# Performance work log

Hardware: AMD Instinct MI355X
Metric: run time of the kernel (lower is better)

The kernel has to match this reference:

```python
import jax, jax.numpy as jnp
import numpy as np

N = 50000      # nodes
E = 800000     # random edges (self loops appended in reference)
B = 500        # graphs
H = 4          # attention heads
F = 64         # feature_dim (per-head out channels)
SLOPE = 0.2    # GATConv leaky_relu negative slope


def gat_layer(x, src, dst, W, att_s, att_d, b):
    # x: [N, Fin]; W: [Fin, H*F]; att_s/att_d: [H, F]; b: [H*F]
    h = (x @ W).reshape(N, H, F)                       # [N,H,F]
    a_s = jnp.einsum('nhf,hf->nh', h, att_s)           # [N,H]
    a_d = jnp.einsum('nhf,hf->nh', h, att_d)           # [N,H]
    e = jax.nn.leaky_relu(a_s[src] + a_d[dst], SLOPE)  # [E',H]
    emax = jax.ops.segment_max(e, dst, num_segments=N) # [N,H] (finite: self loops)
    ee = jnp.exp(e - emax[dst])
    denom = jax.ops.segment_sum(ee, dst, num_segments=N)
    alpha = ee / denom[dst]                            # [E',H]
    out = jax.ops.segment_sum(alpha[:, :, None] * h[src], dst, num_segments=N)
    return out.reshape(N, H * F) + b


def setup_inputs() -> dict:
    key = jax.random.key(0)
    ks = jax.random.split(key, 32)
    s = 0.05
    inp = {
        'node_features': jax.random.normal(ks[0], (N, 5), jnp.float32),
        'building_mask': jax.random.randint(ks[1], (N,), 0, 2),
        'batch': jnp.sort(jax.random.randint(ks[2], (N,), 0, B)),
        'edge_index': jax.random.randint(ks[3], (2, E), 0, N),
        'bbox_W': jax.random.normal(ks[4], (5, 64)) * s,
        'bbox_b': jnp.zeros((64,), jnp.float32),
        'mask_embed': jax.random.normal(ks[5], (2, 64)) * s,
        'node_W': jax.random.normal(ks[6], (128, 64)) * s,
        'node_b': jnp.zeros((64,), jnp.float32),
        'w0': jax.random.normal(ks[7], (64, 256)) * s,
        'as0': jax.random.normal(ks[8], (H, F)) * s,
        'ad0': jax.random.normal(ks[9], (H, F)) * s,
        'b0': jnp.zeros((256,), jnp.float32),
        'w1': jax.random.normal(ks[10], (256, 256)) * s,
        'as1': jax.random.normal(ks[11], (H, F)) * s,
        'ad1': jax.random.normal(ks[12], (H, F)) * s,
        'b1': jnp.zeros((256,), jnp.float32),
        'w2': jax.random.normal(ks[13], (256, 256)) * s,
        'as2': jax.random.normal(ks[14], (H, F)) * s,
        'ad2': jax.random.normal(ks[15], (H, F)) * s,
        'b2': jnp.zeros((256,), jnp.float32),
        'agg_W': jax.random.normal(ks[16], (832, 256)) * s,
        'agg_b': jnp.zeros((256,), jnp.float32),
        'mu_W': jax.random.normal(ks[17], (256, 256)) * s,
        'mu_b': jnp.zeros((256,), jnp.float32),
        'var_W': jax.random.normal(ks[18], (256, 256)) * s,
        'var_b': jnp.zeros((256,), jnp.float32),
    }
    return inp


def reference(node_features, building_mask, batch, edge_index,
              bbox_W, bbox_b, mask_embed, node_W, node_b,
              w0, as0, ad0, b0, w1, as1, ad1, b1, w2, as2, ad2, b2,
              agg_W, agg_b, mu_W, mu_b, var_W, var_b):
    # node featurization
    x = jax.nn.relu(node_features @ bbox_W + bbox_b)          # [N,64]
    m = jax.nn.relu(mask_embed[building_mask])                 # [N,64]
    n0 = jax.nn.relu(jnp.concatenate([x, m], -1) @ node_W + node_b)  # [N,64]

    # self loops (GATConv add_self_loops=True)
    loop = jnp.arange(N, dtype=edge_index.dtype)
    src = jnp.concatenate([edge_index[0], loop])
    dst = jnp.concatenate([edge_index[1], loop])

    g = jax.ops.segment_max(n0, batch, num_segments=B, indices_are_sorted=True)
    g_embed = [g]

    n_t = jax.nn.relu(gat_layer(n0, src, dst, w0, as0, ad0, b0))
    g_embed.append(jax.ops.segment_max(n_t, batch, num_segments=B, indices_are_sorted=True))

    for (W, a_s, a_d, b) in [(w1, as1, ad1, b1), (w2, as2, ad2, b2)]:
        n_t = jax.nn.relu(gat_layer(n_t, src, dst, W, a_s, a_d, b))
        g_embed.append(jax.ops.segment_max(n_t, batch, num_segments=B, indices_are_sorted=True))

    latent = jnp.concatenate(g_embed, -1) @ agg_W + agg_b      # [B,256]
    mu = latent @ mu_W + mu_b
    log_var = latent @ var_W + var_b
    return (mu, log_var)
```

## Files before the change

### kernel.cpp

```cpp
#include <hip/hip_runtime.h>

#define NN 50000
#define EE 800000
#define BB 500
#define SCB 196

typedef short v8s __attribute__((ext_vector_type(8)));
typedef unsigned short v8u __attribute__((ext_vector_type(8)));
typedef float v4f __attribute__((ext_vector_type(4)));

__device__ __forceinline__ float bf2f(unsigned short u) {
    union { unsigned int i; float f; } v; v.i = ((unsigned int)u) << 16; return v.f;
}
__device__ __forceinline__ unsigned short f2bf(float f) {
    union { float f; unsigned int i; } v; v.f = f;
    unsigned int x = v.i;
    unsigned int r = (x + 0x7FFFu + ((x >> 16) & 1u)) >> 16;
    return (unsigned short)r;
}

__device__ __forceinline__ void gll16(const unsigned short* g, v8s* l) {
    __builtin_amdgcn_global_load_lds((const __attribute__((address_space(1))) unsigned int*)g,
                                     (__attribute__((address_space(3))) unsigned int*)l, 16, 0, 0);
}

__global__ void k_sentinel(float* out, float val) {
    int i = blockIdx.x * blockDim.x + threadIdx.x;
    if (i < BB * 512) out[i] = val;
}

__global__ void k_prep(const float* __restrict__ nf, const int* __restrict__ bmask,
                       const float* __restrict__ bboxW, const float* __restrict__ bboxb,
                       const float* __restrict__ membed, unsigned short* __restrict__ feat,
                       const float* __restrict__ a0, unsigned short* __restrict__ d0,
                       const float* __restrict__ a1, unsigned short* __restrict__ d1,
                       const float* __restrict__ a2, unsigned short* __restrict__ d2,
                       const float* __restrict__ a3, unsigned short* __restrict__ d3,
                       int* __restrict__ counts, float* __restrict__ gcat) {
    int g = blockIdx.x * blockDim.x + threadIdx.x;
    if (g < NN) counts[g] = 1;
    if (g < NN * 64) {
        int n = g >> 6, f = g & 63;
        float s = bboxb[f];
        for (int k = 0; k < 5; ++k) s += nf[n * 5 + k] * bboxW[k * 64 + f];
        s = fmaxf(s, 0.f);
        int bm = bmask[n]; if ((unsigned)bm > 1u) bm = 0;
        float mv = fmaxf(membed[bm * 64 + f], 0.f);
        feat[(size_t)n * 128 + f] = f2bf(s);
        feat[(size_t)n * 128 + 64 + f] = f2bf(mv);
        return;
    }
    g -= NN * 64;
    if (g >= 155648) {
        if (g < 155648 + BB * 768) {
            int idx = g - 155648;
            gcat[(idx / 768) * 832 + 64 + (idx % 768)] = 0.f;
        }
        return;
    }
    const float* in; unsigned short* out; int K, Nout, idx;
    if (g < 8192)        { in = a0; out = d0; K = 128; Nout = 64;  idx = g; }
    else if (g < 24576)  { in = a1; out = d1; K = 64;  Nout = 256; idx = g - 8192; }
    else if (g < 90112)  { in = a2; out = d2; K = 256; Nout = 256; idx = g - 24576; }
    else                 { in = a3; out = d3; K = 256; Nout = 256; idx = g - 90112; }
    int k = idx / Nout, n = idx % Nout;
    out[n * K + k] = f2bf(in[idx]);
}

template <int KT, bool BR, bool ATT, int GY>
__global__ __launch_bounds__(256) void k_gemm(const unsigned short* __restrict__ A,
                                              const unsigned short* __restrict__ Bt,
                                              const float* __restrict__ bias,
                                              unsigned short* __restrict__ C, int M, int ldc,
                                              const float* __restrict__ atts, const float* __restrict__ attd,
                                              float* __restrict__ asA, float* __restrict__ adA, int nbx) {
    constexpr int NT = KT / 64;
    constexpr int NB = (NT > 1) ? 2 : 1;
    __shared__ v8s As[NB][512];
    __shared__ v8s Bs[NB][512];
    __shared__ float ap[4][4][4][4][2];
    const int t = threadIdx.x;
    int bx, by;
    if (GY == 4) {
        int p = blockIdx.x;
        int gidx = p >> 5, r = p & 31;
        bx = gidx * 8 + (r & 7);
        by = r >> 3;
        if (bx >= nbx) return;
    } else {
        bx = blockIdx.x; by = 0;
    }
    const int m0 = bx * 64;
    const int n0g = by * 64;
    const int l = t & 63, w = t >> 6;
    const int q = l >> 4, r16 = l & 15;
    const int nloc = w * 16 + r16;

    const int roff0 = (w * 2 + 0) * 8 + (l >> 3);
    const int roff1 = (w * 2 + 1) * 8 + (l >> 3);
    const int kc = (l & 7) ^ (l >> 3);
    const unsigned short* Asrc0 = A + (size_t)(m0 + roff0) * KT + kc * 8;
    const unsigned short* Asrc1 = A + (size_t)(m0 + roff1) * KT + kc * 8;
    const unsigned short* Bsrc0 = Bt + (size_t)(n0g + roff0) * KT + kc * 8;
    const unsigned short* Bsrc1 = Bt + (size_t)(n0g + roff1) * KT + kc * 8;

    v4f acc[4];
#pragma unroll
    for (int i = 0; i < 4; ++i) acc[i] = (v4f){0.f, 0.f, 0.f, 0.f};

    gll16(Asrc0, &As[0][(w * 2 + 0) * 64]);
    gll16(Asrc1, &As[0][(w * 2 + 1) * 64]);
    gll16(Bsrc0, &Bs[0][(w * 2 + 0) * 64]);
    gll16(Bsrc1, &Bs[0][(w * 2 + 1) * 64]);
    __syncthreads();
#pragma unroll
    for (int kt = 0; kt < NT; ++kt) {
        const int b = kt & (NB - 1);
        if (kt + 1 < NT) {
            const int nb = (kt + 1) & (NB - 1);
            gll16(Asrc0 + (kt + 1) * 64, &As[nb][(w * 2 + 0) * 64]);
            gll16(Asrc1 + (kt + 1) * 64, &As[nb][(w * 2 + 1) * 64]);
            gll16(Bsrc0 + (kt + 1) * 64, &Bs[nb][(w * 2 + 0) * 64]);
            gll16(Bsrc1 + (kt + 1) * 64, &Bs[nb][(w * 2 + 1) * 64]);
        }
#pragma unroll
        for (int s = 0; s < 2; ++s) {
            int c = s * 4 + q;
            v8s bfr = Bs[b][nloc * 8 + (c ^ (nloc & 7))];
#pragma unroll
            for (int mt = 0; mt < 4; ++mt) {
                v8s afr = As[b][(mt * 16 + r16) * 8 + (c ^ (r16 & 7))];
                acc[mt] = __builtin_amdgcn_mfma_f32_16x16x32_bf16(afr, bfr, acc[mt], 0, 0, 0);
            }
        }
        __syncthreads();
    }

    const int col = n0g + nloc;
#pragma unroll
    for (int mt = 0; mt < 4; ++mt) {
#pragma unroll
        for (int r = 0; r < 4; ++r) {
            int row = m0 + mt * 16 + q * 4 + r;
            if (row < M) {
                float v = acc[mt][r];
                if (BR) v = fmaxf(v + bias[col], 0.f);
                C[(size_t)row * ldc + col] = f2bf(v);
            }
        }
    }
    if (ATT) {
        float sa = atts[n0g + nloc];
        float da = attd[n0g + nloc];
        float rs[4][4], rd[4][4];
#pragma unroll
        for (int mt = 0; mt < 4; ++mt)
#pragma unroll
            for (int r = 0; r < 4; ++r) { rs[mt][r] = acc[mt][r] * sa; rd[mt][r] = acc[mt][r] * da; }
#pragma unroll
        for (int d = 1; d < 16; d <<= 1) {
#pragma unroll
            for (int mt = 0; mt < 4; ++mt)
#pragma unroll
                for (int r = 0; r < 4; ++r) {
                    rs[mt][r] += __shfl_xor(rs[mt][r], d, 64);
                    rd[mt][r] += __shfl_xor(rd[mt][r], d, 64);
                }
        }
        if (r16 == 0) {
#pragma unroll
            for (int mt = 0; mt < 4; ++mt)
#pragma unroll
                for (int r = 0; r < 4; ++r) { ap[w][q][mt][r][0] = rs[mt][r]; ap[w][q][mt][r][1] = rd[mt][r]; }
        }
        __syncthreads();
        if (t < 128) {
            int row = t >> 1, which = t & 1;
            int qq = (row >> 2) & 3, mtt = row >> 4, rr = row & 3;
            float s = ap[0][qq][mtt][rr][which] + ap[1][qq][mtt][rr][which] +
                      ap[2][qq][mtt][rr][which] + ap[3][qq][mtt][rr][which];
            if (m0 + row < M) (which ? adA : asA)[(m0 + row) * 4 + by] = s;
        }
    }
}

__global__ void k_count(const int* __restrict__ dst, int* __restrict__ counts) {
    int e = blockIdx.x * blockDim.x + threadIdx.x;
    if (e < EE) {
        int d = dst[e];
        if ((unsigned)d < (unsigned)NN) atomicAdd(&counts[d], 1);
    }
}

__global__ __launch_bounds__(256) void k_scanA(const int* __restrict__ counts, int* __restrict__ bsum) {
    __shared__ int red[256];
    const int b = blockIdx.x, t = threadIdx.x;
    int i = b * 256 + t;
    red[t] = (i < NN) ? counts[i] : 0;
    __syncthreads();
    for (int d = 128; d > 0; d >>= 1) {
        if (t < d) red[t] += red[t + d];
        __syncthreads();
    }
    if (t == 0) bsum[b] = red[0];
}

__global__ __launch_bounds__(256) void k_scanB(const int* __restrict__ bsum, int* __restrict__ boff) {
    __shared__ int s[256];
    const int t = threadIdx.x;
    int v = (t < SCB) ? bsum[t] : 0;
    s[t] = v;
    __syncthreads();
    for (int d = 1; d < 256; d <<= 1) {
        int x = (t >= d) ? s[t - d] : 0;
        __syncthreads();
        s[t] += x;
        __syncthreads();
    }
    if (t < SCB) boff[t] = s[t] - v;
}

__global__ __launch_bounds__(256) void k_scanC(const int* __restrict__ counts, const int* __restrict__ boff,
                                               int* __restrict__ off, int* __restrict__ cur) {
    __shared__ int s[256];
    const int b = blockIdx.x, t = threadIdx.x;
    int i = b * 256 + t;
    int v = (i < NN) ? counts[i] : 0;
    s[t] = v;
    __syncthreads();
    for (int d = 1; d < 256; d <<= 1) {
        int x = (t >= d) ? s[t - d] : 0;
        __syncthreads();
        s[t] += x;
        __syncthreads();
    }
    int excl = s[t] - v + boff[b];
    if (i < NN) { off[i] = excl; cur[i] = excl; }
    if (i == NN - 1) off[NN] = excl + v;
}

#define SCAT_K 256
__global__ __launch_bounds__(256) void k_scatter(const int* __restrict__ ei, int* __restrict__ cur,
                                                 int* __restrict__ csr) {
    const int p = blockIdx.x & 7;
    const int j = blockIdx.x >> 3;
    const int plo = p * (NN / 8), phi = plo + (NN / 8);
    const int TOT = EE + NN;
    const int chunk = (TOT + SCAT_K - 1) / SCAT_K;
    const int e1 = min((j + 1) * chunk, TOT);
    for (int e = j * chunk + (int)threadIdx.x; e < e1; e += 256) {
        int d = (e < EE) ? ei[EE + e] : (e - EE);
        if (d < plo || d >= phi) continue;
        int s = (e < EE) ? ei[e] : d;
        if ((unsigned)s >= (unsigned)NN) s = d;
        int pos = atomicAdd(&cur[d], 1);
        csr[pos] = s;
    }
}

__global__ __launch_bounds__(256) void k_agg(const unsigned short* __restrict__ h,
                                             const float* __restrict__ asA, const float* __restrict__ adA,
                                             const int* __restrict__ off, const int* __restrict__ csr,
                                             const float* __restrict__ bias,
                                             unsigned short* __restrict__ nout,
                                             const int* __restrict__ batch,
                                             float* __restrict__ gcat, int gbase) {
    __shared__ int   sL[4][64];
    __shared__ float wL[4][64][4];
    __shared__ float mx[4][256];
    __shared__ int   gb[4];
    const int nd4 = threadIdx.x >> 6;
    const int node = blockIdx.x * 4 + nd4;
    const int l = threadIdx.x & 63;
    const int hl = l >> 4, k16 = l & 15;
    const int o0 = off[node];
    const int deg = off[node + 1] - o0;
    const int dcap = deg < 64 ? deg : 64;
    const float ad4 = adA[node * 4 + hl];
    float sm = 0.f;
    for (int k = k16; k < dcap; k += 16) {
        int s = csr[o0 + k];
        if (hl == 0) sL[nd4][k] = s;
        float e = asA[s * 4 + hl] + ad4;
        e = e > 0.f ? e : 0.2f * e;
        float w = __expf(e);
        wL[nd4][k][hl] = w;
        sm += w;
    }
    for (int k = 64 + k16; k < deg; k += 16) {
        int s = csr[o0 + k];
        float e = asA[s * 4 + hl] + ad4;
        e = e > 0.f ? e : 0.2f * e;
        sm += __expf(e);
    }
#pragma unroll
    for (int d = 1; d < 16; d <<= 1) sm += __shfl_xor(sm, d, 64);
    const float rden = 1.f / sm;
    __syncthreads();
    float a0 = 0.f, a1 = 0.f, a2 = 0.f, a3 = 0.f;
    const int c = l * 4;
    int k = 0;
    for (; k + 4 <= dcap; k += 4) {
        int s0 = sL[nd4][k], s1 = sL[nd4][k + 1], s2 = sL[nd4][k + 2], s3 = sL[nd4][k + 3];
        float w0 = wL[nd4][k][hl], w1 = wL[nd4][k + 1][hl], w2 = wL[nd4][k + 2][hl], w3 = wL[nd4][k + 3][hl];
        ushort4 h0 = *(const ushort4*)(h + (size_t)s0 * 256 + c);
        ushort4 h1 = *(const ushort4*)(h + (size_t)s1 * 256 + c);
        ushort4 h2 = *(const ushort4*)(h + (size_t)s2 * 256 + c);
        ushort4 h3 = *(const ushort4*)(h + (size_t)s3 * 256 + c);
        a0 += w0 * bf2f(h0.x) + w1 * bf2f(h1.x) + w2 * bf2f(h2.x) + w3 * bf2f(h3.x);
        a1 += w0 * bf2f(h0.y) + w1 * bf2f(h1.y) + w2 * bf2f(h2.y) + w3 * bf2f(h3.y);
        a2 += w0 * bf2f(h0.z) + w1 * bf2f(h1.z) + w2 * bf2f(h2.z) + w3 * bf2f(h3.z);
        a3 += w0 * bf2f(h0.w) + w1 * bf2f(h1.w) + w2 * bf2f(h2.w) + w3 * bf2f(h3.w);
    }
    for (; k < dcap; ++k) {
        int s = sL[nd4][k];
        float w = wL[nd4][k][hl];
        ushort4 hv = *(const ushort4*)(h + (size_t)s * 256 + c);
        a0 += w * bf2f(hv.x); a1 += w * bf2f(hv.y); a2 += w * bf2f(hv.z); a3 += w * bf2f(hv.w);
    }
    for (int k2 = 64; k2 < deg; ++k2) {
        int s = csr[o0 + k2];
        float e = asA[s * 4 + hl] + ad4;
        e = e > 0.f ? e : 0.2f * e;
        float w = __expf(e);
        ushort4 hv = *(const ushort4*)(h + (size_t)s * 256 + c);
        a0 += w * bf2f(hv.x); a1 += w * bf2f(hv.y); a2 += w * bf2f(hv.z); a3 += w * bf2f(hv.w);
    }
    float4 bv = *(const float4*)(bias + c);
    float v0 = fmaxf(a0 * rden + bv.x, 0.f);
    float v1 = fmaxf(a1 * rden + bv.y, 0.f);
    float v2 = fmaxf(a2 * rden + bv.z, 0.f);
    float v3 = fmaxf(a3 * rden + bv.w, 0.f);
    ushort4 o;
    o.x = f2bf(v0); o.y = f2bf(v1); o.z = f2bf(v2); o.w = f2bf(v3);
    *(ushort4*)(nout + (size_t)node * 256 + c) = o;

    mx[nd4][c + 0] = v0; mx[nd4][c + 1] = v1; mx[nd4][c + 2] = v2; mx[nd4][c + 3] = v3;
    if (l == 0) gb[nd4] = batch[node];
    __syncthreads();
    const int t = threadIdx.x;
    if (gb[0] == gb[1] && gb[1] == gb[2] && gb[2] == gb[3]) {
        float m = fmaxf(fmaxf(mx[0][t], mx[1][t]), fmaxf(mx[2][t], mx[3][t]));
        atomicMax((int*)(gcat + gb[0] * 832 + gbase + t), __float_as_int(m));
    } else {
        int* g = (int*)(gcat + gb[nd4] * 832 + gbase);
        atomicMax(g + c + 0, __float_as_int(v0));
        atomicMax(g + c + 1, __float_as_int(v1));
        atomicMax(g + c + 2, __float_as_int(v2));
        atomicMax(g + c + 3, __float_as_int(v3));
    }
}

__global__ __launch_bounds__(256) void k_gmaxseg(const unsigned short* __restrict__ nt, int cols,
                                                 const int* __restrict__ batch,
                                                 float* __restrict__ gcat, int gbase) {
    __shared__ float red[256];
    const int b = blockIdx.x, t = threadIdx.x;
    const int lane = t & 63, chunk = t >> 6;
    const int c = blockIdx.y * 64 + lane;
    int lo = 0, hi = NN;
    while (lo < hi) { int mid = (lo + hi) >> 1; if (batch[mid] < b) lo = mid + 1; else hi = mid; }
    int lo2 = lo, hi2 = NN;
    while (lo2 < hi2) { int mid = (lo2 + hi2) >> 1; if (batch[mid] < b + 1) lo2 = mid + 1; else hi2 = mid; }
    float m = 0.f;
    for (int n = lo + chunk; n < lo2; n += 4)
        m = fmaxf(m, bf2f(nt[(size_t)n * cols + c]));
    red[t] = m;
    __syncthreads();
    if (chunk == 0) {
        m = fmaxf(fmaxf(m, red[64 + lane]), fmaxf(red[128 + lane], red[192 + lane]));
        gcat[b * 832 + gbase + c] = m;
    }
}

__global__ __launch_bounds__(256) void k_head1(const float* __restrict__ gcat,
                                               const float* __restrict__ aggW, const float* __restrict__ aggb,
                                               float* __restrict__ latent) {
    __shared__ float gr[832 * 4];
    __shared__ float part[4][4][64];
    const int t = threadIdx.x;
    const int g0 = blockIdx.x * 4, c0 = blockIdx.y * 64;
    for (int i = t; i < 832 * 4; i += 256) {
        int k = i >> 2, g = i & 3;
        gr[i] = gcat[(g0 + g) * 832 + k];
    }
    __syncthreads();
    const int w = t >> 6, l = t & 63;
    const float* wp = aggW + c0 + l;
    float a0 = 0.f, a1 = 0.f, a2 = 0.f, a3 = 0.f;
    const int k0 = w * 208;
#pragma unroll 4
    for (int k = k0; k < k0 + 208; ++k) {
        float wv = wp[(size_t)k * 256];
        float4 gv = *(const float4*)&gr[k * 4];
        a0 += gv.x * wv; a1 += gv.y * wv; a2 += gv.z * wv; a3 += gv.w * wv;
    }
    part[w][0][l] = a0; part[w][1][l] = a1; part[w][2][l] = a2; part[w][3][l] = a3;
    __syncthreads();
    const int g = t >> 6, c = t & 63;
    float s = ((part[0][g][c] + part[1][g][c]) + (part[2][g][c] + part[3][g][c])) + aggb[c0 + c];
    latent[(g0 + g) * 256 + c0 + c] = s;
}

__global__ __launch_bounds__(256) void k_head2(const float* __restrict__ latent,
                                               const float* __restrict__ muW, const float* __restrict__ mub,
                                               const float* __restrict__ vaW, const float* __restrict__ vab,
                                               float* __restrict__ out) {
    __shared__ float lr[256 * 4];
    __shared__ float pm[4][4][64], pv[4][4][64];
    const int t = threadIdx.x;
    const int g0 = blockIdx.x * 4, c0 = blockIdx.y * 64;
    for (int i = t; i < 256 * 4; i += 256) {
        int k = i >> 2, g = i & 3;
        lr[i] = latent[(g0 + g) * 256 + k];
    }
    __syncthreads();
    const int w = t >> 6, l = t & 63;
    const float* mp = muW + c0 + l;
    const float* vp = vaW + c0 + l;
    float m0 = 0.f, m1 = 0.f, m2 = 0.f, m3 = 0.f;
    float v0 = 0.f, v1 = 0.f, v2 = 0.f, v3 = 0.f;
    const int k0 = w * 64;
#pragma unroll 4
    for (int k = k0; k < k0 + 64; ++k) {
        float wm = mp[(size_t)k * 256];
        float wv = vp[(size_t)k * 256];
        float4 gv = *(const float4*)&lr[k * 4];
        m0 += gv.x * wm; m1 += gv.y * wm; m2 += gv.z * wm; m3 += gv.w * wm;
        v0 += gv.x * wv; v1 += gv.y * wv; v2 += gv.z * wv; v3 += gv.w * wv;
    }
    pm[w][0][l] = m0; pm[w][1][l] = m1; pm[w][2][l] = m2; pm[w][3][l] = m3;
    pv[w][0][l] = v0; pv[w][1][l] = v1; pv[w][2][l] = v2; pv[w][3][l] = v3;
    __syncthreads();
    const int g = t >> 6, c = t & 63;
    float smu = ((pm[0][g][c] + pm[1][g][c]) + (pm[2][g][c] + pm[3][g][c])) + mub[c0 + c];
    float sva = ((pv[0][g][c] + pv[1][g][c]) + (pv[2][g][c] + pv[3][g][c])) + vab[c0 + c];
    out[(g0 + g) * 256 + c0 + c] = smu;
    out[BB * 256 + (g0 + g) * 256 + c0 + c] = sva;
}

extern "C" void kernel_launch(void* const* d_in, const int* in_sizes, int n_in,
                              void* d_out, int out_size, void* d_ws, size_t ws_size,
                              hipStream_t stream) {
    (void)in_sizes; (void)n_in; (void)out_size;
    const float* nf     = (const float*)d_in[0];
    const int*   bmask  = (const int*)d_in[1];
    const int*   batch  = (const int*)d_in[2];
    const int*   ei     = (const int*)d_in[3];
    const float* bboxW  = (const float*)d_in[4];
    const float* bboxb  = (const float*)d_in[5];
    const float* membed = (const float*)d_in[6];
    const float* nodeW  = (const float*)d_in[7];
    const float* nodeb  = (const float*)d_in[8];
    const float* w0     = (const float*)d_in[9];
    const float* as0    = (const float*)d_in[10];
    const float* ad0    = (const float*)d_in[11];
    const float* b0     = (const float*)d_in[12];
    const float* w1     = (const float*)d_in[13];
    const float* as1    = (const float*)d_in[14];
    const float* ad1    = (const float*)d_in[15];
    const float* b1     = (const float*)d_in[16];
    const float* w2     = (const float*)d_in[17];
    const float* as2    = (const float*)d_in[18];
    const float* ad2    = (const float*)d_in[19];
    const float* b2     = (const float*)d_in[20];
    const float* aggW   = (const float*)d_in[21];
    const float* aggb   = (const float*)d_in[22];
    const float* muW    = (const float*)d_in[23];
    const float* mub    = (const float*)d_in[24];
    const float* vaW    = (const float*)d_in[25];
    const float* vab    = (const float*)d_in[26];
    float* out = (float*)d_out;

    char* base = (char*)d_ws;
    unsigned short* hbuf    = (unsigned short*)(base);
    unsigned short* nbuf    = (unsigned short*)(base + 25600000);
    unsigned short* feat128 = nbuf;
    unsigned short* n0buf   = (unsigned short*)(base + 25600000 + 12800000);
    char* pool0 = base + 51200000;
    char* p = pool0;
    auto alloc = [&](size_t bytes) { char* r = p; p += (bytes + 255) & ~(size_t)255; return r; };
    unsigned short* nodeWt = (unsigned short*)alloc(128 * 64 * 2);
    unsigned short* w0t    = (unsigned short*)alloc(64 * 256 * 2);
    unsigned short* w1t    = (unsigned short*)alloc(256 * 256 * 2);
    unsigned short* w2t    = (unsigned short*)alloc(256 * 256 * 2);
    float* asA    = (float*)alloc((size_t)NN * 4 * 4);
    float* adA    = (float*)alloc((size_t)NN * 4 * 4);
    int*   counts = (int*)alloc((size_t)NN * 4);
    int*   offs   = (int*)alloc((size_t)(NN + 1) * 4);
    int*   cur    = (int*)alloc((size_t)NN * 4);
    int*   csr    = (int*)alloc((size_t)(EE + NN) * 4);
    float* gcat   = (float*)alloc((size_t)BB * 832 * 4);
    float* latent = (float*)alloc((size_t)BB * 256 * 4);
    int*   bsum   = (int*)alloc(SCB * 4);
    int*   boff   = (int*)alloc(SCB * 4);
    const size_t NEED = (size_t)(p - base);

    if (ws_size < NEED) {
        k_sentinel<<<1000, 256, 0, stream>>>(out, 2000.0f + (float)(ws_size >> 20));
        return;
    }

    k_prep<<<(NN * 64 + 155648 + BB * 768 + 255) / 256, 256, 0, stream>>>(
        nf, bmask, bboxW, bboxb, membed, feat128,
        nodeW, nodeWt, w0, w0t, w1, w1t, w2, w2t, counts, gcat);
    k_count<<<(EE + 255) / 256, 256, 0, stream>>>(ei + EE, counts);
    k_scanA<<<SCB, 256, 0, stream>>>(counts, bsum);
    k_scanB<<<1, 256, 0, stream>>>(bsum, boff);
    k_scanC<<<SCB, 256, 0, stream>>>(counts, boff, offs, cur);
    k_scatter<<<SCAT_K * 8, 256, 0, stream>>>(ei, cur, csr);
    k_gemm<128, true, false, 1><<<782, 256, 0, stream>>>(feat128, nodeWt, nodeb, n0buf, NN, 64,
                                                         nullptr, nullptr, nullptr, nullptr, 782);
    k_gmaxseg<<<dim3(BB, 1), 256, 0, stream>>>(n0buf, 64, batch, gcat, 0);
    k_gemm<64, false, true, 4><<<3136, 256, 0, stream>>>(n0buf, w0t, nullptr, hbuf, NN, 256,
                                                         as0, ad0, asA, adA, 782);
    k_agg<<<12500, 256, 0, stream>>>(hbuf, asA, adA, offs, csr, b0, nbuf, batch, gcat, 64);
    k_gemm<256, false, true, 4><<<3136, 256, 0, stream>>>(nbuf, w1t, nullptr, hbuf, NN, 256,
                                                          as1, ad1, asA, adA, 782);
    k_agg<<<12500, 256, 0, stream>>>(hbuf, asA, adA, offs, csr, b1, nbuf, batch, gcat, 320);
    k_gemm<256, false, true, 4><<<3136, 256, 0, stream>>>(nbuf, w2t, nullptr, hbuf, NN, 256,
                                                          as2, ad2, asA, adA, 782);
    k_agg<<<12500, 256, 0, stream>>>(hbuf, asA, adA, offs, csr, b2, nbuf, batch, gcat, 576);
    k_head1<<<dim3(BB / 4, 4), 256, 0, stream>>>(gcat, aggW, aggb, latent);
    k_head2<<<dim3(BB / 4, 4), 256, 0, stream>>>(latent, muW, mub, vaW, vab, out);
}
```

Measured before the change: 561.3 us.

## Split GAT aggregation into 8 column slices per node with single-pass softmax

```diff
diff --git a/kernel.cpp b/kernel.cpp
--- a/kernel.cpp
+++ b/kernel.cpp
@@ -6,7 +6,6 @@
 #define SCB 196
 
 typedef short v8s __attribute__((ext_vector_type(8)));
-typedef unsigned short v8u __attribute__((ext_vector_type(8)));
 typedef float v4f __attribute__((ext_vector_type(4)));
 
 __device__ __forceinline__ float bf2f(unsigned short u) {
@@ -265,89 +264,52 @@
                                              unsigned short* __restrict__ nout,
                                              const int* __restrict__ batch,
                                              float* __restrict__ gcat, int gbase) {
-    __shared__ int   sL[4][64];
-    __shared__ float wL[4][64][4];
-    __shared__ float mx[4][256];
-    __shared__ int   gb[4];
-    const int nd4 = threadIdx.x >> 6;
-    const int node = blockIdx.x * 4 + nd4;
+    __shared__ float mx[4][32];
+    __shared__ int gb[4];
+    const int p = blockIdx.x & 7;
+    const int wv = threadIdx.x >> 6;
+    const int node = (blockIdx.x >> 3) * 4 + wv;
     const int l = threadIdx.x & 63;
-    const int hl = l >> 4, k16 = l & 15;
+    const int half = l >> 5, li = l & 31;
+    const int col = p * 32 + li;
+    const int hd = p >> 1;
+    const float ad = adA[node * 4 + hd];
     const int o0 = off[node];
     const int deg = off[node + 1] - o0;
-    const int dcap = deg < 64 ? deg : 64;
-    const float ad4 = adA[node * 4 + hl];
-    float sm = 0.f;
-    for (int k = k16; k < dcap; k += 16) {
-        int s = csr[o0 + k];
-        if (hl == 0) sL[nd4][k] = s;
-        float e = asA[s * 4 + hl] + ad4;
+    const unsigned short* hp = h + col;
+
+    float a = 0.f, sm = 0.f;
+    int k = half;
+    int s_n = (k < deg) ? csr[o0 + k] : 0;
+    for (; k < deg; k += 2) {
+        int s = s_n;
+        if (k + 2 < deg) s_n = csr[o0 + k + 2];
+        float as = asA[s * 4 + hd];
+        unsigned short hv = hp[(size_t)s * 256];
+        float e = as + ad;
         e = e > 0.f ? e : 0.2f * e;
         float w = __expf(e);
-        wL[nd4][k][hl] = w;
         sm += w;
-    }
-    for (int k = 64 + k16; k < deg; k += 16) {
-        int s = csr[o0 + k];
-        float e = asA[s * 4 + hl] + ad4;
-        e = e > 0.f ? e : 0.2f * e;
-        sm += __expf(e);
-    }
-#pragma unroll
-    for (int d = 1; d < 16; d <<= 1) sm += __shfl_xor(sm, d, 64);
-    const float rden = 1.f / sm;
-    __syncthreads();
-    float a0 = 0.f, a1 = 0.f, a2 = 0.f, a3 = 0.f;
-    const int c = l * 4;
-    int k = 0;
-    for (; k + 4 <= dcap; k += 4) {
-        int s0 = sL[nd4][k], s1 = sL[nd4][k + 1], s2 = sL[nd4][k + 2], s3 = sL[nd4][k + 3];
-        float w0 = wL[nd4][k][hl], w1 = wL[nd4][k + 1][hl], w2 = wL[nd4][k + 2][hl], w3 = wL[nd4][k + 3][hl];
-        ushort4 h0 = *(const ushort4*)(h + (size_t)s0 * 256 + c);
-        ushort4 h1 = *(const ushort4*)(h + (size_t)s1 * 256 + c);
-        ushort4 h2 = *(const ushort4*)(h + (size_t)s2 * 256 + c);
-        ushort4 h3 = *(const ushort4*)(h + (size_t)s3 * 256 + c);
-        a0 += w0 * bf2f(h0.x) + w1 * bf2f(h1.x) + w2 * bf2f(h2.x) + w3 * bf2f(h3.x);
-        a1 += w0 * bf2f(h0.y) + w1 * bf2f(h1.y) + w2 * bf2f(h2.y) + w3 * bf2f(h3.y);
-        a2 += w0 * bf2f(h0.z) + w1 * bf2f(h1.z) + w2 * bf2f(h2.z) + w3 * bf2f(h3.z);
-        a3 += w0 * bf2f(h0.w) + w1 * bf2f(h1.w) + w2 * bf2f(h2.w) + w3 * bf2f(h3.w);
-    }
-    for (; k < dcap; ++k) {
-        int s = sL[nd4][k];
-        float w = wL[nd4][k][hl];
-        ushort4 hv = *(const ushort4*)(h + (size_t)s * 256 + c);
-        a0 += w * bf2f(hv.x); a1 += w * bf2f(hv.y); a2 += w * bf2f(hv.z); a3 += w * bf2f(hv.w);
-    }
-    for (int k2 = 64; k2 < deg; ++k2) {
-        int s = csr[o0 + k2];
-        float e = asA[s * 4 + hl] + ad4;
-        e = e > 0.f ? e : 0.2f * e;
-        float w = __expf(e);
-        ushort4 hv = *(const ushort4*)(h + (size_t)s * 256 + c);
-        a0 += w * bf2f(hv.x); a1 += w * bf2f(hv.y); a2 += w * bf2f(hv.z); a3 += w * bf2f(hv.w);
-    }
-    float4 bv = *(const float4*)(bias + c);
-    float v0 = fmaxf(a0 * rden + bv.x, 0.f);
-    float v1 = fmaxf(a1 * rden + bv.y, 0.f);
-    float v2 = fmaxf(a2 * rden + bv.z, 0.f);
-    float v3 = fmaxf(a3 * rden + bv.w, 0.f);
-    ushort4 o;
-    o.x = f2bf(v0); o.y = f2bf(v1); o.z = f2bf(v2); o.w = f2bf(v3);
-    *(ushort4*)(nout + (size_t)node * 256 + c) = o;
-
-    mx[nd4][c + 0] = v0; mx[nd4][c + 1] = v1; mx[nd4][c + 2] = v2; mx[nd4][c + 3] = v3;
-    if (l == 0) gb[nd4] = batch[node];
-    __syncthreads();
-    const int t = threadIdx.x;
-    if (gb[0] == gb[1] && gb[1] == gb[2] && gb[2] == gb[3]) {
-        float m = fmaxf(fmaxf(mx[0][t], mx[1][t]), fmaxf(mx[2][t], mx[3][t]));
-        atomicMax((int*)(gcat + gb[0] * 832 + gbase + t), __float_as_int(m));
+        a = fmaf(w, bf2f(hv), a);
+    }
+    a  += __shfl_xor(a, 32, 64);
+    sm += __shfl_xor(sm, 32, 64);
+    const float v = fmaxf(fmaf(a, 1.f / sm, bias[col]), 0.f);
+    if (half == 0) {
+        nout[(size_t)node * 256 + col] = f2bf(v);
+        mx[wv][li] = v;
+    }
+    if (l == 0) gb[wv] = batch[node];
+    __syncthreads();
+    if (gb[0] == gb[3]) {
+        if (threadIdx.x < 32) {
+            float m = fmaxf(fmaxf(mx[0][threadIdx.x], mx[1][threadIdx.x]),
+                            fmaxf(mx[2][threadIdx.x], mx[3][threadIdx.x]));
+            atomicMax((int*)(gcat + gb[0] * 832 + gbase + p * 32 + threadIdx.x), __float_as_int(m));
+        }
     } else {
-        int* g = (int*)(gcat + gb[nd4] * 832 + gbase);
-        atomicMax(g + c + 0, __float_as_int(v0));
-        atomicMax(g + c + 1, __float_as_int(v1));
-        atomicMax(g + c + 2, __float_as_int(v2));
-        atomicMax(g + c + 3, __float_as_int(v3));
+        if (half == 0)
+            atomicMax((int*)(gcat + gb[wv] * 832 + gbase + col), __float_as_int(v));
     }
 }
 
@@ -514,13 +476,13 @@
     k_gmaxseg<<<dim3(BB, 1), 256, 0, stream>>>(n0buf, 64, batch, gcat, 0);
     k_gemm<64, false, true, 4><<<3136, 256, 0, stream>>>(n0buf, w0t, nullptr, hbuf, NN, 256,
                                                          as0, ad0, asA, adA, 782);
-    k_agg<<<12500, 256, 0, stream>>>(hbuf, asA, adA, offs, csr, b0, nbuf, batch, gcat, 64);
+    k_agg<<<12500 * 8, 256, 0, stream>>>(hbuf, asA, adA, offs, csr, b0, nbuf, batch, gcat, 64);
     k_gemm<256, false, true, 4><<<3136, 256, 0, stream>>>(nbuf, w1t, nullptr, hbuf, NN, 256,
                                                           as1, ad1, asA, adA, 782);
-    k_agg<<<12500, 256, 0, stream>>>(hbuf, asA, adA, offs, csr, b1, nbuf, batch, gcat, 320);
+    k_agg<<<12500 * 8, 256, 0, stream>>>(hbuf, asA, adA, offs, csr, b1, nbuf, batch, gcat, 320);
     k_gemm<256, false, true, 4><<<3136, 256, 0, stream>>>(nbuf, w2t, nullptr, hbuf, NN, 256,
                                                           as2, ad2, asA, adA, 782);
-    k_agg<<<12500, 256, 0, stream>>>(hbuf, asA, adA, offs, csr, b2, nbuf, batch, gcat, 576);
+    k_agg<<<12500 * 8, 256, 0, stream>>>(hbuf, asA, adA, offs, csr, b2, nbuf, batch, gcat, 576);
     k_head1<<<dim3(BB / 4, 4), 256, 0, stream>>>(gcat, aggW, aggb, latent);
     k_head2<<<dim3(BB / 4, 4), 256, 0, stream>>>(latent, muW, mub, vaW, vab, out);
 }
```

Measured after the change: 1.201 ms. 114% more time.
